# Performance work log

Hardware: AMD Instinct MI355X
Metric: run time of the kernel (lower is better)

## Reference

```python
import jax, jax.numpy as jnp
import numpy as np

THRESHOLD = 0.5
NEG_RATIO = 3
ALPHA = 1.0
IMG_SIZE = 300.0  # convert_to_ratio divides pixel coords by image size


def _ssd300_default_boxes():
    """Canonical SSD300 priors: 8732 boxes in (cx, cy, w, h), clipped to [0,1]."""
    fmaps = [38, 19, 10, 5, 3, 1]
    scales = [0.1, 0.2, 0.375, 0.55, 0.725, 0.9]
    ars = [[1.0, 2.0, 0.5],
           [1.0, 2.0, 3.0, 0.5, 1.0 / 3.0],
           [1.0, 2.0, 3.0, 0.5, 1.0 / 3.0],
           [1.0, 2.0, 3.0, 0.5, 1.0 / 3.0],
           [1.0, 2.0, 0.5],
           [1.0, 2.0, 0.5]]
    boxes = []
    for k, (f, s) in enumerate(zip(fmaps, scales)):
        for i in range(f):
            for j in range(f):
                cx = (j + 0.5) / f
                cy = (i + 0.5) / f
                for ar in ars[k]:
                    boxes.append([cx, cy, s * np.sqrt(ar), s / np.sqrt(ar)])
                    if ar == 1.0:
                        s2 = np.sqrt(s * scales[k + 1]) if k < len(fmaps) - 1 else 1.0
                        boxes.append([cx, cy, s2, s2])
    return np.clip(np.asarray(boxes, dtype=np.float32), 0.0, 1.0)  # (8732, 4)


def _cxcy_to_xy(b):
    return jnp.concatenate([b[..., :2] - b[..., 2:] / 2.0,
                            b[..., :2] + b[..., 2:] / 2.0], axis=-1)


def _iou(a, b):
    # a: [N,4] xyxy, b: [P,4] xyxy -> [N,P]
    lt = jnp.maximum(a[:, None, :2], b[None, :, :2])
    rb = jnp.minimum(a[:, None, 2:], b[None, :, 2:])
    wh = jnp.clip(rb - lt, 0.0)
    inter = wh[..., 0] * wh[..., 1]
    area_a = (a[:, 2] - a[:, 0]) * (a[:, 3] - a[:, 1])
    area_b = (b[:, 2] - b[:, 0]) * (b[:, 3] - b[:, 1])
    return inter / (area_a[:, None] + area_b[None, :] - inter)


def _encode_cxcy(t, d):
    # standard SSD offsets (variances 0.1, 0.2). Safe log for unmatched (zero) boxes
    # -- those entries are masked out of the loss, matching torch's positive-only gather.
    g_cxcy = (t[..., :2] - d[..., :2]) / (d[..., 2:] / 10.0)
    safe_wh = jnp.where(t[..., 2:] > 0.0, t[..., 2:], d[..., 2:])
    g_wh = jnp.log(safe_wh / d[..., 2:]) * 5.0
    return jnp.concatenate([g_cxcy, g_wh], axis=-1)


def setup_inputs() -> dict:
    key = jax.random.key(0)
    k1, k2, k3, k4 = jax.random.split(key, 4)
    B, P, C, N = 128, 8732, 81, 16
    predicted_boxes = jax.random.normal(k1, (B, P, 4), dtype=jnp.float32)
    predicted_scores = jax.random.normal(k2, (B, P, C), dtype=jnp.float32)
    u = jax.random.uniform(k3, (B, N, 4), dtype=jnp.float32)
    cxcy = (0.15 + 0.7 * u[..., :2]) * IMG_SIZE   # centers in pixel coords
    wh = (0.08 + 0.32 * u[..., 2:]) * IMG_SIZE    # sizes in pixel coords
    target_boxes = jnp.concatenate([cxcy, wh], axis=-1)
    target_labels = jax.random.randint(k4, (B, N), 1, C)
    default_boxes = jnp.asarray(_ssd300_default_boxes())
    return {"predicted_boxes": predicted_boxes,
            "predicted_scores": predicted_scores,
            "target_boxes": target_boxes,
            "target_labels": target_labels,
            "default_boxes": default_boxes}


def reference(predicted_boxes, predicted_scores, target_boxes, target_labels, default_boxes):
    B, P, C = predicted_scores.shape
    db_xy = _cxcy_to_xy(default_boxes)
    tb = target_boxes / IMG_SIZE  # convert_to_ratio

    def match(boxes, labels):
        # boxes: [N,4] cxcywh (ratio), labels: [N]
        ov = _iou(_cxcy_to_xy(boxes), db_xy)          # [N, P]
        best_ov = ov.max(axis=0)                      # [P]
        obj_idx = ov.argmax(axis=0)                   # [P]
        box_idx = ov.argmax(axis=1)                   # [N] best prior per object
        obj_idx = obj_idx.at[box_idx].set(jnp.arange(boxes.shape[0]))
        check = best_ov > THRESHOLD                   # uses pre-scatter max (faithful)
        t_lab = jnp.where(check, labels[obj_idx], 0)
        t_box = jnp.where(check[:, None], boxes[obj_idx], 0.0)
        return _encode_cxcy(t_box, default_boxes), t_lab

    true_bboxes, true_labels = jax.vmap(match)(tb, target_labels)  # [B,P,4], [B,P]

    positive = true_labels != 0                        # [B,P]
    n_pos = jnp.maximum(positive.sum(), 1)

    # SmoothL1 (beta=1), mean over positive elements (num_pos * 4)
    diff = jnp.abs(predicted_boxes - true_bboxes)
    sl1 = jnp.where(diff < 1.0, 0.5 * diff * diff, diff - 0.5)
    bbox_loss = (sl1 * positive[..., None]).sum() / (n_pos.astype(sl1.dtype) * 4.0)

    # per-box cross entropy
    logp = jax.nn.log_softmax(predicted_scores, axis=-1)
    cls_all = -jnp.take_along_axis(logp, true_labels[..., None], axis=-1)[..., 0]  # [B,P]

    cls_pos_sum = (cls_all * positive).sum()
    neg = jnp.where(positive, 0.0, cls_all)
    neg_sorted = -jnp.sort(-neg, axis=1)               # descending per image
    n_hard = positive.sum(axis=1) * NEG_RATIO          # [B]
    rank = jnp.arange(P)[None, :]
    hard_neg_sum = (neg_sorted * (rank < n_hard[:, None])).sum()

    cls_loss = (cls_pos_sum + hard_neg_sum) / n_pos.astype(cls_all.dtype)
    return cls_loss + ALPHA * bbox_loss
```

## Files before the change

### kernel.cpp

```cpp
#include <hip/hip_runtime.h>
#include <hip/hip_bf16.h>
#include <math.h>

#define BB 128
#define PP 8732
#define NN 16
#define CC 81
#define IMG 300.0f
#define TILE_ROWS 64
#define NT ((BB * PP) / TILE_ROWS)
#define K1_THREADS 512

__global__ __launch_bounds__(K1_THREADS) void k1_match(
    const float* __restrict__ pred_boxes,
    const float* __restrict__ tgt_boxes,
    const int*   __restrict__ tgt_labels,
    const float* __restrict__ dboxes,
    int*   __restrict__ tlab_out,
    float* __restrict__ bbox_partial,
    int*   __restrict__ pos_count)
{
    const int b   = blockIdx.x;
    const int tid = threadIdx.x;
    const int NW  = K1_THREADS / 64;

    __shared__ float t_cx[NN], t_cy[NN], t_w[NN], t_h[NN];
    __shared__ float t_x0s[NN], t_y0s[NN], t_x1s[NN], t_y1s[NN], t_areas[NN];
    __shared__ int   t_lab[NN];
    __shared__ unsigned short obj_s[PP];
    __shared__ unsigned char  chk_s[PP];
    __shared__ float red_v[NN][NW];
    __shared__ int   red_i[NN][NW];
    __shared__ int   box_idx_s[NN];
    __shared__ float red_f[NW];
    __shared__ int   red_c[NW];

    if (tid < NN) {
        const float* tb = tgt_boxes + ((size_t)b * NN + tid) * 4;
        float cx = tb[0] / IMG, cy = tb[1] / IMG, w = tb[2] / IMG, h = tb[3] / IMG;
        t_cx[tid] = cx; t_cy[tid] = cy; t_w[tid] = w; t_h[tid] = h;
        float x0 = cx - w * 0.5f, y0 = cy - h * 0.5f;
        float x1 = cx + w * 0.5f, y1 = cy + h * 0.5f;
        t_x0s[tid] = x0; t_y0s[tid] = y0; t_x1s[tid] = x1; t_y1s[tid] = y1;
        t_areas[tid] = (x1 - x0) * (y1 - y0);
        t_lab[tid] = tgt_labels[(size_t)b * NN + tid];
    }
    __syncthreads();

    float tx0[NN], ty0[NN], tx1[NN], ty1[NN], tar[NN];
#pragma unroll
    for (int n = 0; n < NN; ++n) {
        tx0[n] = t_x0s[n]; ty0[n] = t_y0s[n];
        tx1[n] = t_x1s[n]; ty1[n] = t_y1s[n];
        tar[n] = t_areas[n];
    }

    float bestv[NN];
    int   bestp[NN];
#pragma unroll
    for (int n = 0; n < NN; ++n) { bestv[n] = -1e30f; bestp[n] = 0x7fffffff; }

    for (int p = tid; p < PP; p += K1_THREADS) {
        float4 d = *reinterpret_cast<const float4*>(dboxes + (size_t)p * 4);
        float dx0 = d.x - d.z * 0.5f, dy0 = d.y - d.w * 0.5f;
        float dx1 = d.x + d.z * 0.5f, dy1 = d.y + d.w * 0.5f;
        float dar = (dx1 - dx0) * (dy1 - dy0);
        float bov = -1.0f; int bidx = 0;
#pragma unroll
        for (int n = 0; n < NN; ++n) {
            float lx = fmaxf(tx0[n], dx0);
            float ly = fmaxf(ty0[n], dy0);
            float rx = fminf(tx1[n], dx1);
            float ry = fminf(ty1[n], dy1);
            float iw = fmaxf(rx - lx, 0.0f);
            float ih = fmaxf(ry - ly, 0.0f);
            float inter = iw * ih;
            float iou = inter / (tar[n] + dar - inter);
            if (iou > bov) { bov = iou; bidx = n; }
            if (iou > bestv[n]) { bestv[n] = iou; bestp[n] = p; }
        }
        obj_s[p] = (unsigned short)bidx;
        chk_s[p] = (bov > 0.5f) ? 1 : 0;
    }

#pragma unroll
    for (int n = 0; n < NN; ++n) {
        float v = bestv[n]; int ip = bestp[n];
        for (int off = 32; off; off >>= 1) {
            float v2 = __shfl_xor(v, off);
            int   p2 = __shfl_xor(ip, off);
            if (v2 > v || (v2 == v && p2 < ip)) { v = v2; ip = p2; }
        }
        if ((tid & 63) == 0) { red_v[n][tid >> 6] = v; red_i[n][tid >> 6] = ip; }
    }
    __syncthreads();
    if (tid < NN) {
        float v = red_v[tid][0]; int ip = red_i[tid][0];
        for (int w = 1; w < NW; ++w) {
            float v2 = red_v[tid][w]; int p2 = red_i[tid][w];
            if (v2 > v || (v2 == v && p2 < ip)) { v = v2; ip = p2; }
        }
        box_idx_s[tid] = ip;
    }
    __syncthreads();
    if (tid == 0) {
        for (int n = 0; n < NN; ++n) obj_s[box_idx_s[n]] = (unsigned short)n;
    }
    __syncthreads();

    float bacc = 0.0f;
    int   pcnt = 0;
    for (int p = tid; p < PP; p += K1_THREADS) {
        int lab = 0;
        if (chk_s[p]) {
            int n = obj_s[p];
            lab = t_lab[n];
            if (lab != 0) {
                ++pcnt;
                float4 d = *reinterpret_cast<const float4*>(dboxes + (size_t)p * 4);
                float gx = (t_cx[n] - d.x) / (d.z / 10.0f);
                float gy = (t_cy[n] - d.y) / (d.w / 10.0f);
                float gw = logf(t_w[n] / d.z) * 5.0f;
                float gh = logf(t_h[n] / d.w) * 5.0f;
                float4 pv = *reinterpret_cast<const float4*>(pred_boxes + ((size_t)b * PP + p) * 4);
                float dfs[4] = { pv.x - gx, pv.y - gy, pv.z - gw, pv.w - gh };
#pragma unroll
                for (int j = 0; j < 4; ++j) {
                    float ad = fabsf(dfs[j]);
                    bacc += (ad < 1.0f) ? 0.5f * ad * ad : ad - 0.5f;
                }
            }
        }
        tlab_out[(size_t)b * PP + p] = lab;
    }
    for (int off = 32; off; off >>= 1) {
        bacc += __shfl_xor(bacc, off);
        pcnt += __shfl_xor(pcnt, off);
    }
    if ((tid & 63) == 0) { red_f[tid >> 6] = bacc; red_c[tid >> 6] = pcnt; }
    __syncthreads();
    if (tid == 0) {
        float s = 0.0f; int c = 0;
        for (int w = 0; w < NW; ++w) { s += red_f[w]; c += red_c[w]; }
        bbox_partial[b] = s;
        pos_count[b]    = c;
    }
}

__global__ __launch_bounds__(256) void k2_cls(
    const float* __restrict__ scores,
    const int*   __restrict__ tlab,
    float* __restrict__ neg,
    float* __restrict__ clspos_partial)
{
    __shared__ float slds[TILE_ROWS * CC];
    const int tid = threadIdx.x;
    const int t   = blockIdx.x;

    const float* g = scores + (size_t)t * (TILE_ROWS * CC);
    for (int i = tid; i < TILE_ROWS * CC; i += 256)
        slds[i] = g[i];
    __syncthreads();

    const int row = tid >> 2;
    const int q   = tid & 3;
    const float* myrow = &slds[row * CC];
    const int base = q * 20;

    float x[21];
#pragma unroll
    for (int i = 0; i < 20; ++i) x[i] = myrow[base + i];
    x[20] = (q == 3) ? myrow[80] : -1e30f;

    float m = x[0];
#pragma unroll
    for (int i = 1; i < 21; ++i) m = fmaxf(m, x[i]);
    m = fmaxf(m, __shfl_xor(m, 1));
    m = fmaxf(m, __shfl_xor(m, 2));

    float s0 = 0.0f, s1 = 0.0f, s2 = 0.0f, s3 = 0.0f;
#pragma unroll
    for (int i = 0; i < 20; i += 4) {
        s0 += __expf(x[i + 0] - m);
        s1 += __expf(x[i + 1] - m);
        s2 += __expf(x[i + 2] - m);
        s3 += __expf(x[i + 3] - m);
    }
    s0 += __expf(x[20] - m);
    float s = (s0 + s1) + (s2 + s3);
    s += __shfl_xor(s, 1);
    s += __shfl_xor(s, 2);

    float acc = 0.0f;
    if (q == 0) {
        long long r = (long long)t * TILE_ROWS + row;
        int   lab = tlab[r];
        float cls = m + __logf(s) - slds[row * CC + lab];
        if (lab != 0) { acc = cls; neg[r] = 0.0f; }
        else          { neg[r] = cls; }
    }

    for (int off = 32; off; off >>= 1) acc += __shfl_xor(acc, off);
    __shared__ float wsum[4];
    if ((tid & 63) == 0) wsum[tid >> 6] = acc;
    __syncthreads();
    if (tid == 0)
        clspos_partial[t] = wsum[0] + wsum[1] + wsum[2] + wsum[3];
}

__global__ __launch_bounds__(256) void k3_topk(
    const float* __restrict__ neg,
    const int*   __restrict__ pos_count,
    float* __restrict__ hard_partial)
{
    const int b   = blockIdx.x;
    const int tid = threadIdx.x;

    __shared__ unsigned int vals[PP];
    __shared__ int hist[256];
    __shared__ int scan[256];
    __shared__ unsigned int s_prefix;
    __shared__ int s_kk;
    __shared__ float wsum[4];

    for (int i = tid; i < PP; i += 256)
        vals[i] = __float_as_uint(neg[(size_t)b * PP + i]);

    int k = pos_count[b] * 3;
    if (k > PP) k = PP;
    if (k <= 0) {
        if (tid == 0) hard_partial[b] = 0.0f;
        return;
    }
    if (tid == 0) { s_prefix = 0u; s_kk = k; }
    __syncthreads();

    unsigned int prefmask = 0u;
    for (int round = 0; round < 4; ++round) {
        const int shift = 24 - 8 * round;
        hist[tid] = 0;
        __syncthreads();
        unsigned int pref = s_prefix;
        for (int i = tid; i < PP; i += 256) {
            unsigned int v = vals[i];
            if ((v & prefmask) == pref)
                atomicAdd(&hist[(v >> shift) & 0xFF], 1);
        }
        __syncthreads();
        scan[tid] = hist[tid];
        __syncthreads();
        for (int off = 1; off < 256; off <<= 1) {
            int add = (tid + off < 256) ? scan[tid + off] : 0;
            __syncthreads();
            scan[tid] += add;
            __syncthreads();
        }
        int sg = scan[tid] - hist[tid];
        int kk = s_kk;
        __syncthreads();
        if (sg < kk && sg + hist[tid] >= kk) {
            s_prefix = pref | ((unsigned int)tid << shift);
            s_kk     = kk - sg;
        }
        __syncthreads();
        prefmask |= (0xFFu << shift);
    }

    unsigned int t = s_prefix;
    int kk = s_kk;
    float tf = __uint_as_float(t);

    float acc = 0.0f;
    for (int i = tid; i < PP; i += 256) {
        unsigned int v = vals[i];
        if (v > t) acc += __uint_as_float(v);
    }
    for (int off = 32; off; off >>= 1) acc += __shfl_xor(acc, off);
    if ((tid & 63) == 0) wsum[tid >> 6] = acc;
    __syncthreads();
    if (tid == 0)
        hard_partial[b] = wsum[0] + wsum[1] + wsum[2] + wsum[3] + (float)kk * tf;
}

__global__ __launch_bounds__(256) void k4_final(
    const float* __restrict__ clspos_partial,
    const float* __restrict__ bbox_partial,
    const float* __restrict__ hard_partial,
    const int*   __restrict__ pos_count,
    float* __restrict__ out)
{
    const int tid = threadIdx.x;
    float cacc = 0.0f, bacc = 0.0f, hacc = 0.0f;
    int   pacc = 0;
    for (int i = tid; i < NT; i += 256) cacc += clspos_partial[i];
    if (tid < BB) {
        bacc = bbox_partial[tid];
        hacc = hard_partial[tid];
        pacc = pos_count[tid];
    }
    __shared__ float sc[256], sb[256], sh[256];
    __shared__ int   sp[256];
    sc[tid] = cacc; sb[tid] = bacc; sh[tid] = hacc; sp[tid] = pacc;
    __syncthreads();
    for (int off = 128; off; off >>= 1) {
        if (tid < off) {
            sc[tid] += sc[tid + off];
            sb[tid] += sb[tid + off];
            sh[tid] += sh[tid + off];
            sp[tid] += sp[tid + off];
        }
        __syncthreads();
    }
    if (tid == 0) {
        float npos = fmaxf((float)sp[0], 1.0f);
        out[0] = (sc[0] + sh[0]) / npos + sb[0] / (npos * 4.0f);
    }
}

extern "C" void kernel_launch(void* const* d_in, const int* in_sizes, int n_in,
                              void* d_out, int out_size, void* d_ws, size_t ws_size,
                              hipStream_t stream) {
    const float* pred_boxes  = (const float*)d_in[0];
    const float* pred_scores = (const float*)d_in[1];
    const float* tgt_boxes   = (const float*)d_in[2];
    const int*   tgt_labels  = (const int*)d_in[3];
    const float* dboxes      = (const float*)d_in[4];
    float* out = (float*)d_out;

    char* ws = (char*)d_ws;
    int*   tlab           = (int*)ws;   ws += (size_t)BB * PP * sizeof(int);
    float* neg            = (float*)ws; ws += (size_t)BB * PP * sizeof(float);
    int*   pos_count      = (int*)ws;   ws += BB * sizeof(int);
    float* bbox_partial   = (float*)ws; ws += BB * sizeof(float);
    float* hard_partial   = (float*)ws; ws += BB * sizeof(float);
    float* clspos_partial = (float*)ws; ws += (size_t)NT * sizeof(float);

    k1_match<<<BB, K1_THREADS, 0, stream>>>(pred_boxes, tgt_boxes, tgt_labels, dboxes,
                                            tlab, bbox_partial, pos_count);
    k2_cls<<<NT, 256, 0, stream>>>(pred_scores, tlab, neg, clspos_partial);
    k3_topk<<<BB, 256, 0, stream>>>(neg, pos_count, hard_partial);
    k4_final<<<1, 256, 0, stream>>>(clspos_partial, bbox_partial, hard_partial,
                                    pos_count, out);
}
```

Baseline: 159.5 us.

## Fuse final reduction into top-k kernel and speed up radix-select scan

Merges the final reduction kernel into the top-k kernel using a global atomic completion counter, so the last block to finish performs the final sum and one launch is removed. The top-k kernel moves to 512 threads and replaces the barrier-heavy Hillis-Steele scan with wave-level shuffle scans plus a small cross-wave total. The score tile load in the cross-entropy kernel is vectorized to float4. The counter is reset by the first kernel, which adds a dependency on launch ordering and on threadfence correctness.

Result: slower. 168.3 us (+5.5%).

```diff
diff --git a/kernel.cpp b/kernel.cpp
--- a/kernel.cpp
+++ b/kernel.cpp
@@ -10,6 +10,7 @@
 #define TILE_ROWS 64
 #define NT ((BB * PP) / TILE_ROWS)
 #define K1_THREADS 512
+#define K3_THREADS 512
 
 __global__ __launch_bounds__(K1_THREADS) void k1_match(
     const float* __restrict__ pred_boxes,
@@ -18,11 +19,14 @@
     const float* __restrict__ dboxes,
     int*   __restrict__ tlab_out,
     float* __restrict__ bbox_partial,
-    int*   __restrict__ pos_count)
+    int*   __restrict__ pos_count,
+    int*   __restrict__ k3_done)
 {
     const int b   = blockIdx.x;
     const int tid = threadIdx.x;
     const int NW  = K1_THREADS / 64;
+
+    if (b == 0 && tid == 0) *k3_done = 0;
 
     __shared__ float t_cx[NN], t_cy[NN], t_w[NN], t_h[NN];
     __shared__ float t_x0s[NN], t_y0s[NN], t_x1s[NN], t_y1s[NN], t_areas[NN];
@@ -157,9 +161,10 @@
     const int tid = threadIdx.x;
     const int t   = blockIdx.x;
 
-    const float* g = scores + (size_t)t * (TILE_ROWS * CC);
-    for (int i = tid; i < TILE_ROWS * CC; i += 256)
-        slds[i] = g[i];
+    const float4* g4 = reinterpret_cast<const float4*>(scores + (size_t)t * (TILE_ROWS * CC));
+    float4* s4 = reinterpret_cast<float4*>(slds);
+    for (int i = tid; i < (TILE_ROWS * CC) / 4; i += 256)
+        s4[i] = g4[i];
     __syncthreads();
 
     const int row = tid >> 2;
@@ -208,101 +213,116 @@
         clspos_partial[t] = wsum[0] + wsum[1] + wsum[2] + wsum[3];
 }
 
-__global__ __launch_bounds__(256) void k3_topk(
+__global__ __launch_bounds__(K3_THREADS) void k3_topk_final(
     const float* __restrict__ neg,
     const int*   __restrict__ pos_count,
-    float* __restrict__ hard_partial)
+    const float* __restrict__ clspos_partial,
+    const float* __restrict__ bbox_partial,
+    float* __restrict__ hard_partial,
+    int*   __restrict__ done,
+    float* __restrict__ out)
 {
-    const int b   = blockIdx.x;
-    const int tid = threadIdx.x;
+    const int b    = blockIdx.x;
+    const int tid  = threadIdx.x;
+    const int lane = tid & 63;
+    const int wv   = tid >> 6;
 
     __shared__ unsigned int vals[PP];
     __shared__ int hist[256];
-    __shared__ int scan[256];
+    __shared__ int waveTot[4];
     __shared__ unsigned int s_prefix;
     __shared__ int s_kk;
-    __shared__ float wsum[4];
-
-    for (int i = tid; i < PP; i += 256)
+    __shared__ float wsum[8];
+    __shared__ int s_last;
+
+    for (int i = tid; i < PP; i += K3_THREADS)
         vals[i] = __float_as_uint(neg[(size_t)b * PP + i]);
 
     int k = pos_count[b] * 3;
     if (k > PP) k = PP;
-    if (k <= 0) {
-        if (tid == 0) hard_partial[b] = 0.0f;
-        return;
-    }
-    if (tid == 0) { s_prefix = 0u; s_kk = k; }
-    __syncthreads();
-
-    unsigned int prefmask = 0u;
-    for (int round = 0; round < 4; ++round) {
-        const int shift = 24 - 8 * round;
-        hist[tid] = 0;
+    float hp = 0.0f;
+
+    if (k > 0) {
+        if (tid == 0) { s_prefix = 0u; s_kk = k; }
         __syncthreads();
-        unsigned int pref = s_prefix;
-        for (int i = tid; i < PP; i += 256) {
+
+        unsigned int prefmask = 0u;
+        for (int round = 0; round < 4; ++round) {
+            const int shift = 24 - 8 * round;
+            if (tid < 256) hist[tid] = 0;
+            __syncthreads();
+            const unsigned int pref = s_prefix;
+            const int kkR = s_kk;
+            for (int i = tid; i < PP; i += K3_THREADS) {
+                unsigned int v = vals[i];
+                if ((v & prefmask) == pref)
+                    atomicAdd(&hist[(v >> shift) & 0xFF], 1);
+            }
+            __syncthreads();
+            if (tid < 256) {
+                int myh = hist[tid];
+                int s = myh;
+#pragma unroll
+                for (int off = 1; off < 64; off <<= 1) {
+                    int v = __shfl_down(s, off);
+                    if (lane + off < 64) s += v;
+                }
+                if (lane == 0) waveTot[wv] = s;
+                __syncthreads();
+                int addhi = 0;
+                for (int w2 = wv + 1; w2 < 4; ++w2) addhi += waveTot[w2];
+                s += addhi;
+                int sg = s - myh;
+                if (sg < kkR && sg + myh >= kkR) {
+                    s_prefix = pref | ((unsigned int)tid << shift);
+                    s_kk     = kkR - sg;
+                }
+            } else {
+                __syncthreads();
+            }
+            prefmask |= (0xFFu << shift);
+        }
+        __syncthreads();
+
+        const unsigned int t = s_prefix;
+        const int kk = s_kk;
+        const float tf = __uint_as_float(t);
+
+        float acc = 0.0f;
+        for (int i = tid; i < PP; i += K3_THREADS) {
             unsigned int v = vals[i];
-            if ((v & prefmask) == pref)
-                atomicAdd(&hist[(v >> shift) & 0xFF], 1);
-        }
+            if (v > t) acc += __uint_as_float(v);
+        }
+        for (int off = 32; off; off >>= 1) acc += __shfl_xor(acc, off);
+        if (lane == 0) wsum[wv] = acc;
         __syncthreads();
-        scan[tid] = hist[tid];
-        __syncthreads();
-        for (int off = 1; off < 256; off <<= 1) {
-            int add = (tid + off < 256) ? scan[tid + off] : 0;
-            __syncthreads();
-            scan[tid] += add;
-            __syncthreads();
-        }
-        int sg = scan[tid] - hist[tid];
-        int kk = s_kk;
-        __syncthreads();
-        if (sg < kk && sg + hist[tid] >= kk) {
-            s_prefix = pref | ((unsigned int)tid << shift);
-            s_kk     = kk - sg;
-        }
-        __syncthreads();
-        prefmask |= (0xFFu << shift);
-    }
-
-    unsigned int t = s_prefix;
-    int kk = s_kk;
-    float tf = __uint_as_float(t);
-
-    float acc = 0.0f;
-    for (int i = tid; i < PP; i += 256) {
-        unsigned int v = vals[i];
-        if (v > t) acc += __uint_as_float(v);
-    }
-    for (int off = 32; off; off >>= 1) acc += __shfl_xor(acc, off);
-    if ((tid & 63) == 0) wsum[tid >> 6] = acc;
-    __syncthreads();
-    if (tid == 0)
-        hard_partial[b] = wsum[0] + wsum[1] + wsum[2] + wsum[3] + (float)kk * tf;
-}
-
-__global__ __launch_bounds__(256) void k4_final(
-    const float* __restrict__ clspos_partial,
-    const float* __restrict__ bbox_partial,
-    const float* __restrict__ hard_partial,
-    const int*   __restrict__ pos_count,
-    float* __restrict__ out)
-{
-    const int tid = threadIdx.x;
+        if (tid == 0) {
+            float ssum = 0.0f;
+            for (int w = 0; w < 8; ++w) ssum += wsum[w];
+            hp = ssum + (float)kk * tf;
+        }
+    }
+    if (tid == 0) hard_partial[b] = hp;
+
+    __threadfence();
+    if (tid == 0) s_last = (atomicAdd(done, 1) == BB - 1) ? 1 : 0;
+    __syncthreads();
+    if (!s_last) return;
+    __threadfence();
+
     float cacc = 0.0f, bacc = 0.0f, hacc = 0.0f;
     int   pacc = 0;
-    for (int i = tid; i < NT; i += 256) cacc += clspos_partial[i];
+    for (int i = tid; i < NT; i += K3_THREADS) cacc += clspos_partial[i];
     if (tid < BB) {
         bacc = bbox_partial[tid];
         hacc = hard_partial[tid];
         pacc = pos_count[tid];
     }
-    __shared__ float sc[256], sb[256], sh[256];
-    __shared__ int   sp[256];
+    __shared__ float sc[K3_THREADS], sb[K3_THREADS], sh[K3_THREADS];
+    __shared__ int   sp[K3_THREADS];
     sc[tid] = cacc; sb[tid] = bacc; sh[tid] = hacc; sp[tid] = pacc;
     __syncthreads();
-    for (int off = 128; off; off >>= 1) {
+    for (int off = K3_THREADS / 2; off; off >>= 1) {
         if (tid < off) {
             sc[tid] += sc[tid + off];
             sb[tid] += sb[tid + off];
@@ -333,12 +353,13 @@
     int*   pos_count      = (int*)ws;   ws += BB * sizeof(int);
     float* bbox_partial   = (float*)ws; ws += BB * sizeof(float);
     float* hard_partial   = (float*)ws; ws += BB * sizeof(float);
+    int*   k3_done        = (int*)ws;   ws += 4 * sizeof(int);
     float* clspos_partial = (float*)ws; ws += (size_t)NT * sizeof(float);
 
     k1_match<<<BB, K1_THREADS, 0, stream>>>(pred_boxes, tgt_boxes, tgt_labels, dboxes,
-                                            tlab, bbox_partial, pos_count);
+                                            tlab, bbox_partial, pos_count, k3_done);
     k2_cls<<<NT, 256, 0, stream>>>(pred_scores, tlab, neg, clspos_partial);
-    k3_topk<<<BB, 256, 0, stream>>>(neg, pos_count, hard_partial);
-    k4_final<<<1, 256, 0, stream>>>(clspos_partial, bbox_partial, hard_partial,
-                                    pos_count, out);
+    k3_topk_final<<<BB, K3_THREADS, 0, stream>>>(neg, pos_count, clspos_partial,
+                                                 bbox_partial, hard_partial,
+                                                 k3_done, out);
 }
```
